# Kernel tuning notes

Measured on AMD Instinct MI355X. Metric: run time of the kernel, lower is better.

## Reference

```python
import jax, jax.numpy as jnp
import numpy as np
import math

D_MODEL = 1024
N_HEADS = 16
D_HEAD = D_MODEL // N_HEADS


def setup_inputs() -> dict:
    key = jax.random.key(0)
    k_x, k_wqkv, k_bqkv, k_wp, k_bp = jax.random.split(key, 5)
    B, T = 2, 2048
    s = 1.0 / math.sqrt(D_MODEL)
    return {
        "x": jax.random.normal(k_x, (B, T, D_MODEL), dtype=jnp.float32),
        "W_qkv": jax.random.uniform(k_wqkv, (D_MODEL, 3 * D_MODEL), minval=-s, maxval=s, dtype=jnp.float32),
        "b_qkv": jax.random.uniform(k_bqkv, (3 * D_MODEL,), minval=-s, maxval=s, dtype=jnp.float32),
        "W_proj": jax.random.uniform(k_wp, (D_MODEL, D_MODEL), minval=-s, maxval=s, dtype=jnp.float32),
        "b_proj": jax.random.uniform(k_bp, (D_MODEL,), minval=-s, maxval=s, dtype=jnp.float32),
    }


def reference(x, W_qkv, b_qkv, W_proj, b_proj):
    B, T, C = x.shape
    qkv = x @ W_qkv + b_qkv                      # [B,T,3C]
    qkv = qkv.reshape(B, T, 3, N_HEADS, D_HEAD)
    qkv = jnp.transpose(qkv, (2, 0, 3, 1, 4))     # [3,B,H,T,dh]
    q, k, v = qkv[0], qkv[1], qkv[2]
    scale = math.sqrt(D_HEAD)
    attn = jnp.einsum('bhqd,bhkd->bhqk', q, k) / scale  # [B,H,T,T]
    causal = jnp.tril(jnp.ones((T, T), dtype=bool))
    attn = jnp.where(causal, attn, -jnp.inf)
    attn = jax.nn.softmax(attn, axis=-1)
    out = jnp.einsum('bhqk,bhkd->bhqd', attn, v)  # [B,H,T,dh]
    out = jnp.transpose(out, (0, 2, 1, 3)).reshape(B, T, C)
    return out @ W_proj + b_proj
```

## Files before the change

### kernel.cpp

```cpp
#include <hip/hip_runtime.h>

#define B_    2
#define T_    2048
#define C_    1024
#define H_    16
#define DH_   64
#define M_    (B_ * T_)
#define NQKV  (3 * C_)

typedef __bf16 bf16;
typedef __bf16 bf16x2 __attribute__((ext_vector_type(2)));
typedef __bf16 bf16x4 __attribute__((ext_vector_type(4)));
typedef __bf16 bf16x8 __attribute__((ext_vector_type(8)));
typedef float  f32x4  __attribute__((ext_vector_type(4)));
typedef float  f32x16 __attribute__((ext_vector_type(16)));
typedef unsigned u32x4 __attribute__((ext_vector_type(4)));

__device__ __forceinline__ void async16(const void* g, void* l) {
  __builtin_amdgcn_global_load_lds(
      (const __attribute__((address_space(1))) void*)g,
      (__attribute__((address_space(3))) void*)l, 16, 0, 0);
}

__device__ __forceinline__ unsigned pk(float a, float b) {
  bf16x2 t; t[0] = (bf16)a; t[1] = (bf16)b;
  return __builtin_bit_cast(unsigned, t);
}

__global__ __launch_bounds__(256) void prep_k(
    const float* __restrict__ x, bf16* __restrict__ xbf,
    const float* __restrict__ Wqkv, bf16* __restrict__ wqkvT,
    const float* __restrict__ Wproj, bf16* __restrict__ wprojT) {
  __shared__ float tile[32][33];
  const int bid = blockIdx.x;
  if (bid < 4096) {
    const int i = (bid * 256 + threadIdx.x) * 4;
    float4 v = *(const float4*)(x + i);
    bf16x4 o;
    o[0] = (bf16)v.x; o[1] = (bf16)v.y; o[2] = (bf16)v.z; o[3] = (bf16)v.w;
    *(bf16x4*)(xbf + i) = o;
    return;
  }
  const float* in; bf16* out; int R, C, cb, rb;
  if (bid < 4096 + 3072) {
    const int b = bid - 4096;
    in = Wqkv; out = wqkvT; R = 1024; C = 3072; cb = b % 96; rb = b / 96;
  } else {
    const int b = bid - 7168;
    in = Wproj; out = wprojT; R = 1024; C = 1024; cb = b & 31; rb = b >> 5;
  }
  const int c0 = cb * 32, r0 = rb * 32;
  const int tx = threadIdx.x & 31, ty = threadIdx.x >> 5;
#pragma unroll
  for (int j = 0; j < 4; j++)
    tile[ty + j * 8][tx] = in[(size_t)(r0 + ty + j * 8) * C + c0 + tx];
  __syncthreads();
#pragma unroll
  for (int j = 0; j < 4; j++)
    out[(size_t)(c0 + ty + j * 8) * R + r0 + tx] = (bf16)tile[tx][ty + j * 8];
}

template <int EPI, int BM>
__global__ __launch_bounds__(256) void gemm_k(
    const bf16* __restrict__ A, const bf16* __restrict__ Bt,
    const float* __restrict__ bias, float* __restrict__ outF,
    bf16* __restrict__ qb, bf16* __restrict__ kb, bf16* __restrict__ vtb) {
  constexpr int K = 1024;
  constexpr int MI = BM / 32;
  __shared__ alignas(16) bf16 As[BM * 64];
  __shared__ alignas(16) bf16 Bs[128 * 64];
  const int tid = threadIdx.x;
  const int lane = tid & 63, wv = tid >> 6;
  const int l15 = lane & 15, quad = lane >> 4;
  const int wm = (wv >> 1) * (BM / 2), wn = (wv & 1) * 64;
  const int m0 = blockIdx.x * BM, n0 = blockIdx.y * 128;

  f32x4 acc[MI][4] = {};

  const int srow = tid >> 3;
  const int sgb = ((tid & 7) ^ (srow & 7)) * 8;
  const bf16* ga = A + (size_t)(m0 + srow) * K + sgb;
  const bf16* gb = Bt + (size_t)(n0 + srow) * K + sgb;
  const int swz = l15 & 7;

  for (int it = 0; it < K / 64; ++it) {
    const int k0 = it * 64;
#pragma unroll
    for (int c = 0; c < BM / 32; c++)
      async16(ga + k0 + (size_t)(c * 32) * K, As + tid * 8 + c * 2048);
#pragma unroll
    for (int c = 0; c < 4; c++)
      async16(gb + k0 + (size_t)(c * 32) * K, Bs + tid * 8 + c * 2048);
    __syncthreads();
    bf16x8 af[2][MI], bfr[2][4];
#pragma unroll
    for (int kk = 0; kk < 2; kk++) {
#pragma unroll
      for (int i = 0; i < MI; i++)
        af[kk][i] = *(const bf16x8*)(As + (wm + i * 16 + l15) * 64 +
                                     (((kk * 4 + quad) ^ swz) << 3));
#pragma unroll
      for (int j = 0; j < 4; j++)
        bfr[kk][j] = *(const bf16x8*)(Bs + (wn + j * 16 + l15) * 64 +
                                      (((kk * 4 + quad) ^ swz) << 3));
    }
#pragma unroll
    for (int kk = 0; kk < 2; kk++)
#pragma unroll
      for (int i = 0; i < MI; i++)
#pragma unroll
        for (int j = 0; j < 4; j++)
          acc[i][j] = __builtin_amdgcn_mfma_f32_16x16x32_bf16(
              af[kk][i], bfr[kk][j], acc[i][j], 0, 0, 0);
    __syncthreads();
  }

#pragma unroll
  for (int i = 0; i < MI; i++) {
#pragma unroll
    for (int j = 0; j < 4; j++) {
      const int gcol = n0 + wn + j * 16 + l15;
      const float bv = bias[gcol];
      const int trow = m0 + wm + i * 16 + quad * 4;
      if constexpr (EPI == 0) {
        const int which = gcol >> 10;
        const int hn = gcol & 1023;
        const int h = hn >> 6, d = hn & 63;
        const int bb = trow >> 11, t = trow & 2047;
        const int head = bb * 16 + h;
        if (which == 0) {
#pragma unroll
          for (int r = 0; r < 4; r++)
            qb[head * 131072 + (t + r) * 64 + d] =
                (bf16)((acc[i][j][r] + bv) * 0.1803368801f);
        } else if (which == 1) {
#pragma unroll
          for (int r = 0; r < 4; r++)
            kb[head * 131072 + (t + r) * 64 + d] = (bf16)(acc[i][j][r] + bv);
        } else {
          bf16x4 pv;
#pragma unroll
          for (int r = 0; r < 4; r++) pv[r] = (bf16)(acc[i][j][r] + bv);
          *(bf16x4*)(vtb + head * 131072 + d * 2048 + t) = pv;
        }
      } else {
#pragma unroll
        for (int r = 0; r < 4; r++)
          outF[(size_t)(trow + r) * 1024 + gcol] = acc[i][j][r] + bv;
      }
    }
  }
}

__global__ __launch_bounds__(256, 2) void attn_k(const bf16* __restrict__ Q,
                                                 const bf16* __restrict__ K,
                                                 const bf16* __restrict__ Vt,
                                                 bf16* __restrict__ O) {
  __shared__ alignas(16) bf16 Ks[2][128 * 64];
  __shared__ alignas(16) bf16 Vs[2][64 * 128];
  const int tid = threadIdx.x, lane = tid & 63, wv = tid >> 6;
  const int l31 = lane & 31, hi = lane >> 5;

  const int b = blockIdx.x;
  const int sH = b >> 8, i = b & 255;
  const int bh = (i & 7) | (((i >> 3) & 3) << 3);
  const int x = i >> 5;
  const int qJ = sH ? (15 - x) : x;
  const int q0 = qJ * 128;
  const int nIter = qJ + 1;

  const bf16* Qb = Q + (size_t)bh * 131072;
  const bf16* Kb = K + (size_t)bh * 131072;
  const bf16* Vb = Vt + (size_t)bh * 131072;

  const int krow = tid >> 3;
  const int kg = (tid & 7) ^ (krow & 7);
  const bf16* gk = Kb + krow * 64 + kg * 8;
  const int vrow = tid >> 4;
  const int vg = (tid & 15) ^ (vrow & 15);
  const bf16* gv = Vb + vrow * 2048 + vg * 8;

  const int swzk = l31 & 7;
  const int swzv = l31 & 15;
  const int bb = bh >> 4, h = bh & 15;

  const int q = q0 + wv * 32 + l31;
  bf16x8 aq[4];
#pragma unroll
  for (int ds = 0; ds < 4; ds++)
    aq[ds] = *(const bf16x8*)(Qb + q * 64 + ds * 16 + hi * 8);

  f32x16 o0 = {}, o1 = {};
  float m = -3.0e38f, lsum = 0.f;

#pragma unroll
  for (int c = 0; c < 4; c++) {
    async16(gk + c * (32 * 64), &Ks[0][tid * 8 + c * 2048]);
    async16(gv + c * (16 * 2048), &Vs[0][tid * 8 + c * 2048]);
  }

  for (int it = 0; it < nIter; ++it) {
    const int cur = it & 1;
    __syncthreads();
    if (it + 1 < nIter) {
      const int kt1 = (it + 1) * 128;
#pragma unroll
      for (int c = 0; c < 4; c++) {
        async16(gk + kt1 * 64 + c * (32 * 64), &Ks[cur ^ 1][tid * 8 + c * 2048]);
        async16(gv + kt1 + c * (16 * 2048), &Vs[cur ^ 1][tid * 8 + c * 2048]);
      }
    }
    const bf16* Kc = Ks[cur];
    const bf16* Vc = Vs[cur];

    f32x16 s[4] = {};
    __builtin_amdgcn_s_setprio(1);
#pragma unroll
    for (int nf = 0; nf < 4; nf++) {
      const int row = nf * 32 + l31;
#pragma unroll
      for (int ds = 0; ds < 4; ds++) {
        bf16x8 kf = *(const bf16x8*)(Kc + row * 64 + (((ds * 2 + hi) ^ swzk) << 3));
        s[nf] = __builtin_amdgcn_mfma_f32_32x32x16_bf16(kf, aq[ds], s[nf], 0, 0, 0);
      }
    }
    __builtin_amdgcn_s_setprio(0);

    if (it == nIter - 1) {
#pragma unroll
      for (int nf = 0; nf < 4; nf++)
#pragma unroll
        for (int r = 0; r < 16; r++) {
          const int kt = it * 128 + nf * 32 + (r & 3) + 8 * (r >> 2) + 4 * hi;
          if (kt > q) s[nf][r] = -3.0e38f;
        }
    }

    float mx = s[0][0];
#pragma unroll
    for (int nf = 0; nf < 4; nf++)
#pragma unroll
      for (int r = 0; r < 16; r++) mx = fmaxf(mx, s[nf][r]);
    mx = fmaxf(mx, __shfl_xor(mx, 32));
    if (!__all(mx - m <= 8.0f)) {
      const float mnew = fmaxf(m, mx);
      const float alpha = __builtin_amdgcn_exp2f(m - mnew);
      m = mnew; lsum *= alpha;
#pragma unroll
      for (int r = 0; r < 16; r++) { o0[r] *= alpha; o1[r] *= alpha; }
    }
    float ts = 0.f;
    unsigned w[4][8];
#pragma unroll
    for (int nf = 0; nf < 4; nf++)
#pragma unroll
      for (int k = 0; k < 8; k++) {
        const float pa = __builtin_amdgcn_exp2f(s[nf][2 * k] - m);
        const float pc = __builtin_amdgcn_exp2f(s[nf][2 * k + 1] - m);
        ts += pa + pc;
        w[nf][k] = pk(pa, pc);
      }
    ts += __shfl_xor(ts, 32);
    lsum += ts;

    __builtin_amdgcn_s_setprio(1);
#pragma unroll
    for (int nf = 0; nf < 4; nf++) {
#pragma unroll
      for (int half = 0; half < 2; half++) {
        const unsigned w0 = w[nf][half * 4 + 0], w1 = w[nf][half * 4 + 1];
        const unsigned w2 = w[nf][half * 4 + 2], w3 = w[nf][half * 4 + 3];
        const unsigned rx = (unsigned)__shfl_xor((int)(hi ? w0 : w2), 32);
        const unsigned ry = (unsigned)__shfl_xor((int)(hi ? w1 : w3), 32);
        u32x4 pw;
        pw[0] = hi ? rx : w0;
        pw[1] = hi ? ry : w1;
        pw[2] = hi ? w2 : rx;
        pw[3] = hi ? w3 : ry;
        const bf16x8 pb = __builtin_bit_cast(bf16x8, pw);
        const int c = nf * 2 + half;
        const bf16x8 vf0 = *(const bf16x8*)(Vc + l31 * 128 +
                                            (((c * 2 + hi) ^ swzv) << 3));
        o0 = __builtin_amdgcn_mfma_f32_32x32x16_bf16(vf0, pb, o0, 0, 0, 0);
        const bf16x8 vf1 = *(const bf16x8*)(Vc + (32 + l31) * 128 +
                                            (((c * 2 + hi) ^ swzv) << 3));
        o1 = __builtin_amdgcn_mfma_f32_32x32x16_bf16(vf1, pb, o1, 0, 0, 0);
      }
    }
    __builtin_amdgcn_s_setprio(0);
  }

  const float inv = 1.0f / lsum;
  bf16* Op = O + (size_t)(bb * 2048 + q) * 1024 + h * 64;
#pragma unroll
  for (int g = 0; g < 4; g++) {
    bf16x4 v0, v1;
#pragma unroll
    for (int k = 0; k < 4; k++) {
      v0[k] = (bf16)(o0[g * 4 + k] * inv);
      v1[k] = (bf16)(o1[g * 4 + k] * inv);
    }
    *(bf16x4*)(Op + g * 8 + hi * 4) = v0;
    *(bf16x4*)(Op + 32 + g * 8 + hi * 4) = v1;
  }
}

extern "C" void kernel_launch(void* const* d_in, const int* in_sizes, int n_in,
                              void* d_out, int out_size, void* d_ws, size_t ws_size,
                              hipStream_t stream) {
  const float* x     = (const float*)d_in[0];
  const float* Wqkv  = (const float*)d_in[1];
  const float* bqkv  = (const float*)d_in[2];
  const float* Wproj = (const float*)d_in[3];
  const float* bproj = (const float*)d_in[4];
  float* out = (float*)d_out;

  char* p = (char*)d_ws;
  bf16* xbf    = (bf16*)p; p += (size_t)M_ * C_ * 2;
  bf16* wqkvT  = (bf16*)p; p += (size_t)NQKV * C_ * 2;
  bf16* wprojT = (bf16*)p; p += (size_t)C_ * C_ * 2;
  bf16* Qb     = (bf16*)p; p += (size_t)M_ * C_ * 2;
  bf16* Kb     = (bf16*)p; p += (size_t)M_ * C_ * 2;
  bf16* Vtb    = (bf16*)p; p += (size_t)M_ * C_ * 2;
  bf16* AO     = (bf16*)p;

  prep_k<<<8192, 256, 0, stream>>>(x, xbf, Wqkv, wqkvT, Wproj, wprojT);

  gemm_k<0, 64><<<dim3(M_ / 64, NQKV / 128), 256, 0, stream>>>(
      xbf, wqkvT, bqkv, nullptr, Qb, Kb, Vtb);

  attn_k<<<512, 256, 0, stream>>>(Qb, Kb, Vtb, AO);

  gemm_k<1, 64><<<dim3(M_ / 64, C_ / 128), 256, 0, stream>>>(
      AO, wprojT, bproj, out, nullptr, nullptr, nullptr);
}
```

Measured before the change: 173.6 us.

## Split attention key tiles across two wave groups and merge softmax partials

The attention kernel now runs 512 threads per block: each of the four query slices is handled by two waves, each processing half of the 128-key tile (split-K within a block). Each wave keeps its own running max, sum and output accumulator, and at the end the partials are merged through shared memory with a log-sum-exp rescale before writing. The aim is more waves per CU and shorter per-wave dependency chains to hide MFMA and exp latency. The row max and sum reductions are also turned into trees. In exchange the merge adds an extra barrier and shared-memory traffic, and the launch bounds of 512 threads with 4 blocks tighten the register budget.

```diff
diff --git a/kernel.cpp b/kernel.cpp
--- a/kernel.cpp
+++ b/kernel.cpp
@@ -152,7 +152,7 @@
   }
 }
 
-__global__ __launch_bounds__(256, 2) void attn_k(const bf16* __restrict__ Q,
+__global__ __launch_bounds__(512, 4) void attn_k(const bf16* __restrict__ Q,
                                                  const bf16* __restrict__ K,
                                                  const bf16* __restrict__ Vt,
                                                  bf16* __restrict__ O) {
@@ -160,6 +160,7 @@
   __shared__ alignas(16) bf16 Vs[2][64 * 128];
   const int tid = threadIdx.x, lane = tid & 63, wv = tid >> 6;
   const int l31 = lane & 31, hi = lane >> 5;
+  const int qs = wv & 3, halfw = wv >> 2;
 
   const int b = blockIdx.x;
   const int sH = b >> 8, i = b & 255;
@@ -184,7 +185,7 @@
   const int swzv = l31 & 15;
   const int bb = bh >> 4, h = bh & 15;
 
-  const int q = q0 + wv * 32 + l31;
+  const int q = q0 + qs * 32 + l31;
   bf16x8 aq[4];
 #pragma unroll
   for (int ds = 0; ds < 4; ds++)
@@ -194,9 +195,9 @@
   float m = -3.0e38f, lsum = 0.f;
 
 #pragma unroll
-  for (int c = 0; c < 4; c++) {
-    async16(gk + c * (32 * 64), &Ks[0][tid * 8 + c * 2048]);
-    async16(gv + c * (16 * 2048), &Vs[0][tid * 8 + c * 2048]);
+  for (int c = 0; c < 2; c++) {
+    async16(gk + c * (64 * 64), &Ks[0][tid * 8 + c * 4096]);
+    async16(gv + c * (32 * 2048), &Vs[0][tid * 8 + c * 4096]);
   }
 
   for (int it = 0; it < nIter; ++it) {
@@ -205,19 +206,19 @@
     if (it + 1 < nIter) {
       const int kt1 = (it + 1) * 128;
 #pragma unroll
-      for (int c = 0; c < 4; c++) {
-        async16(gk + kt1 * 64 + c * (32 * 64), &Ks[cur ^ 1][tid * 8 + c * 2048]);
-        async16(gv + kt1 + c * (16 * 2048), &Vs[cur ^ 1][tid * 8 + c * 2048]);
+      for (int c = 0; c < 2; c++) {
+        async16(gk + kt1 * 64 + c * (64 * 64), &Ks[cur ^ 1][tid * 8 + c * 4096]);
+        async16(gv + kt1 + c * (32 * 2048), &Vs[cur ^ 1][tid * 8 + c * 4096]);
       }
     }
     const bf16* Kc = Ks[cur];
     const bf16* Vc = Vs[cur];
 
-    f32x16 s[4] = {};
+    f32x16 s[2] = {};
     __builtin_amdgcn_s_setprio(1);
 #pragma unroll
-    for (int nf = 0; nf < 4; nf++) {
-      const int row = nf * 32 + l31;
+    for (int nf = 0; nf < 2; nf++) {
+      const int row = halfw * 64 + nf * 32 + l31;
 #pragma unroll
       for (int ds = 0; ds < 4; ds++) {
         bf16x8 kf = *(const bf16x8*)(Kc + row * 64 + (((ds * 2 + hi) ^ swzk) << 3));
@@ -228,19 +229,25 @@
 
     if (it == nIter - 1) {
 #pragma unroll
-      for (int nf = 0; nf < 4; nf++)
+      for (int nf = 0; nf < 2; nf++)
 #pragma unroll
         for (int r = 0; r < 16; r++) {
-          const int kt = it * 128 + nf * 32 + (r & 3) + 8 * (r >> 2) + 4 * hi;
+          const int kt = it * 128 + halfw * 64 + nf * 32 +
+                         (r & 3) + 8 * (r >> 2) + 4 * hi;
           if (kt > q) s[nf][r] = -3.0e38f;
         }
     }
 
-    float mx = s[0][0];
-#pragma unroll
-    for (int nf = 0; nf < 4; nf++)
-#pragma unroll
-      for (int r = 0; r < 16; r++) mx = fmaxf(mx, s[nf][r]);
+    float red[8];
+#pragma unroll
+    for (int r = 0; r < 8; r++)
+      red[r] = fmaxf(fmaxf(s[0][r], s[0][r + 8]), fmaxf(s[1][r], s[1][r + 8]));
+#pragma unroll
+    for (int st = 4; st >= 1; st >>= 1)
+#pragma unroll
+      for (int r = 0; r < 4; r++)
+        if (r < st) red[r] = fmaxf(red[r], red[r + st]);
+    float mx = red[0];
     mx = fmaxf(mx, __shfl_xor(mx, 32));
     if (!__all(mx - m <= 8.0f)) {
       const float mnew = fmaxf(m, mx);
@@ -249,27 +256,28 @@
 #pragma unroll
       for (int r = 0; r < 16; r++) { o0[r] *= alpha; o1[r] *= alpha; }
     }
-    float ts = 0.f;
-    unsigned w[4][8];
-#pragma unroll
-    for (int nf = 0; nf < 4; nf++)
+    float tsp[4] = {0.f, 0.f, 0.f, 0.f};
+    unsigned w[2][8];
+#pragma unroll
+    for (int nf = 0; nf < 2; nf++)
 #pragma unroll
       for (int k = 0; k < 8; k++) {
         const float pa = __builtin_amdgcn_exp2f(s[nf][2 * k] - m);
         const float pc = __builtin_amdgcn_exp2f(s[nf][2 * k + 1] - m);
-        ts += pa + pc;
+        tsp[k & 3] += pa + pc;
         w[nf][k] = pk(pa, pc);
       }
+    float ts = (tsp[0] + tsp[1]) + (tsp[2] + tsp[3]);
     ts += __shfl_xor(ts, 32);
     lsum += ts;
 
     __builtin_amdgcn_s_setprio(1);
 #pragma unroll
-    for (int nf = 0; nf < 4; nf++) {
-#pragma unroll
-      for (int half = 0; half < 2; half++) {
-        const unsigned w0 = w[nf][half * 4 + 0], w1 = w[nf][half * 4 + 1];
-        const unsigned w2 = w[nf][half * 4 + 2], w3 = w[nf][half * 4 + 3];
+    for (int nf = 0; nf < 2; nf++) {
+#pragma unroll
+      for (int hh = 0; hh < 2; hh++) {
+        const unsigned w0 = w[nf][hh * 4 + 0], w1 = w[nf][hh * 4 + 1];
+        const unsigned w2 = w[nf][hh * 4 + 2], w3 = w[nf][hh * 4 + 3];
         const unsigned rx = (unsigned)__shfl_xor((int)(hi ? w0 : w2), 32);
         const unsigned ry = (unsigned)__shfl_xor((int)(hi ? w1 : w3), 32);
         u32x4 pw;
@@ -278,7 +286,7 @@
         pw[2] = hi ? w2 : rx;
         pw[3] = hi ? w3 : ry;
         const bf16x8 pb = __builtin_bit_cast(bf16x8, pw);
-        const int c = nf * 2 + half;
+        const int c = halfw * 4 + nf * 2 + hh;
         const bf16x8 vf0 = *(const bf16x8*)(Vc + l31 * 128 +
                                             (((c * 2 + hi) ^ swzv) << 3));
         o0 = __builtin_amdgcn_mfma_f32_32x32x16_bf16(vf0, pb, o0, 0, 0, 0);
@@ -290,18 +298,39 @@
     __builtin_amdgcn_s_setprio(0);
   }
 
-  const float inv = 1.0f / lsum;
-  bf16* Op = O + (size_t)(bb * 2048 + q) * 1024 + h * 64;
-#pragma unroll
-  for (int g = 0; g < 4; g++) {
-    bf16x4 v0, v1;
-#pragma unroll
-    for (int k = 0; k < 4; k++) {
-      v0[k] = (bf16)(o0[g * 4 + k] * inv);
-      v1[k] = (bf16)(o1[g * 4 + k] * inv);
-    }
-    *(bf16x4*)(Op + g * 8 + hi * 4) = v0;
-    *(bf16x4*)(Op + 32 + g * 8 + hi * 4) = v1;
+  __syncthreads();
+  float* oX = (float*)Vs;
+  float* mX = (float*)Ks;
+  const int slot = qs * 64 + lane;
+  if (halfw == 1) {
+#pragma unroll
+    for (int r = 0; r < 16; r++) {
+      oX[r * 256 + slot] = o0[r];
+      oX[(16 + r) * 256 + slot] = o1[r];
+    }
+    mX[slot] = m;
+    mX[256 + slot] = lsum;
+  }
+  __syncthreads();
+  if (halfw == 0) {
+    const float mB = mX[slot], lB = mX[256 + slot];
+    const float m12 = fmaxf(m, mB);
+    const float aA = __builtin_amdgcn_exp2f(m - m12);
+    const float aB = __builtin_amdgcn_exp2f(mB - m12);
+    const float inv = 1.0f / (lsum * aA + lB * aB);
+    bf16* Op = O + (size_t)(bb * 2048 + q) * 1024 + h * 64;
+#pragma unroll
+    for (int g = 0; g < 4; g++) {
+      bf16x4 v0, v1;
+#pragma unroll
+      for (int k2 = 0; k2 < 4; k2++) {
+        const int r = g * 4 + k2;
+        v0[k2] = (bf16)((o0[r] * aA + oX[r * 256 + slot] * aB) * inv);
+        v1[k2] = (bf16)((o1[r] * aA + oX[(16 + r) * 256 + slot] * aB) * inv);
+      }
+      *(bf16x4*)(Op + g * 8 + hi * 4) = v0;
+      *(bf16x4*)(Op + 32 + g * 8 + hi * 4) = v1;
+    }
   }
 }
 
@@ -329,7 +358,7 @@
   gemm_k<0, 64><<<dim3(M_ / 64, NQKV / 128), 256, 0, stream>>>(
       xbf, wqkvT, bqkv, nullptr, Qb, Kb, Vtb);
 
-  attn_k<<<512, 256, 0, stream>>>(Qb, Kb, Vtb, AO);
+  attn_k<<<512, 512, 0, stream>>>(Qb, Kb, Vtb, AO);
 
   gemm_k<1, 64><<<dim3(M_ / 64, C_ / 128), 256, 0, stream>>>(
       AO, wprojT, bproj, out, nullptr, nullptr, nullptr);
```

Measured after the change: 170.9 us. No clear change (-1.6%).
